# Optimization experiments

Measured on AMD Instinct MI355X. Metric: run time of the kernel, lower is better.

Reference implementation:

```python
import jax, jax.numpy as jnp
import numpy as np

BS, SEQ = 32, 48
VOCAB, H, IMG_F = 32529, 512, 4096
EPS = 1e-5


def setup_inputs() -> dict:
    key = jax.random.key(0)
    ks = jax.random.split(key, 24)
    stdv = 1.0 / np.sqrt(H)
    u = lambda k, shp, s=stdv: jax.random.uniform(k, shp, jnp.float32, -s, s)
    inp = {
        'img': jax.random.normal(ks[0], (BS, IMG_F), jnp.float32),
        'x': jax.random.randint(ks[1], (BS, SEQ), 0, VOCAB),
        # CNN (all convs are kernel-size-1 -> plain linears)
        'w1': u(ks[2], (2048, IMG_F)), 'b1': u(ks[3], (2048,)),
        'g1': jnp.ones((2048,)), 'be1': jnp.zeros((2048,)),
        'w2': u(ks[4], (1024, 2048)), 'b2': u(ks[5], (1024,)),
        'g2': jnp.ones((1024,)), 'be2': jnp.zeros((1024,)),
        'w3': u(ks[6], (H, 1024)), 'b3': u(ks[7], (H,)),
        'g3': jnp.ones((H,)), 'be3': jnp.zeros((H,)),
        # LSTM gates stacked in order i, f, g(c), o
        'U': u(ks[8], (H, 4 * H)),
        'V': u(ks[9], (H, 4 * H)),
        'bg': u(ks[10], (4 * H,)),
        'emb': u(ks[11], (VOCAB, H)),
        'Wout': u(ks[12], (H, VOCAB)),
        'bout': u(ks[13], (VOCAB,)),
    }
    return inp


def _bn(h, g, b):
    # BatchNorm1d in training mode over batch dim (spatial length is 1)
    mu = h.mean(0)
    v = jnp.var(h, 0)
    return g * (h - mu) * jax.lax.rsqrt(v + EPS) + b


def _cnn(img, w1, b1, g1, be1, w2, b2, g2, be2, w3, b3, g3, be3):
    h = jax.nn.relu(_bn(img @ w1.T + b1, g1, be1))
    h = jax.nn.relu(_bn(h @ w2.T + b2, g2, be2))
    h = jax.nn.relu(_bn(h @ w3.T + b3, g3, be3))
    return h  # [bs, 512]


def _lstm(feat, xe, U, V, bg):
    bs = feat.shape[0]
    h = jnp.zeros((bs, H), feat.dtype)
    c = jnp.zeros((bs, H), feat.dtype)

    def gates(z, c):
        z = z.reshape(bs, 4, H)
        i = jax.nn.sigmoid(z[:, 0])
        f = jax.nn.sigmoid(z[:, 1])
        g = jnp.tanh(z[:, 2])
        o = jax.nn.sigmoid(z[:, 3])
        c = f * c + i * g
        return o * jnp.tanh(c), c

    # image step: feat is added identically to every gate pre-activation
    z0 = feat[:, None, :].repeat(4, 1).reshape(bs, 4 * H) + h @ V + bg
    h, c = gates(z0, c)

    # precompute all input projections in one GEMM: [seq, bs, 4H]
    xU = jnp.einsum('bsh,hk->sbk', xe, U)

    def step(carry, xu):
        h, c = carry
        h, c = gates(xu + h @ V + bg, c)
        return (h, c), h

    (h, c), hs = jax.lax.scan(step, (h, c), xU)
    return hs.transpose(1, 0, 2), h, c  # [bs, seq, H]


def reference(img, x, w1, b1, g1, be1, w2, b2, g2, be2, w3, b3, g3, be3,
              U, V, bg, emb, Wout, bout):
    feat = _cnn(img, w1, b1, g1, be1, w2, b2, g2, be2, w3, b3, g3, be3)
    xe = emb[x]  # [bs, seq, H]
    hs, h, c = _lstm(feat, xe, U, V, bg)
    logits = hs @ Wout + bout  # [bs, seq, vocab]
    seq_pred = jax.nn.softmax(logits, axis=2)
    return seq_pred, (h, c)
```

## Files before the change

kernel.cpp:

```cpp
#include <hip/hip_runtime.h>
#include <stdint.h>

#define BS 32
#define SEQ 48
#define VOCAB 32529
#define HD 512
#define IMG_F 4096
#define EPS 1e-5f
#define NPAD16 2040

typedef __attribute__((ext_vector_type(8))) short short8;
typedef __attribute__((ext_vector_type(4))) float f32x4;

#define MFMA(a, b, c) __builtin_amdgcn_mfma_f32_16x16x32_bf16(a, b, c, 0, 0, 0)

static __device__ __forceinline__ unsigned short f2bf(float v) {
  union { float f; unsigned u; } c; c.f = v;
  unsigned r = (c.u + 0x7FFFu + ((c.u >> 16) & 1u)) >> 16;
  return (unsigned short)r;
}
static __device__ __forceinline__ float bf2f(unsigned short h) {
  union { unsigned u; float f; } c; c.u = ((unsigned)h) << 16; return c.f;
}
static __device__ __forceinline__ float sigf(float x) {
  x = fminf(fmaxf(x, -30.f), 30.f);
  return 1.f / (1.f + __expf(-x));
}
static __device__ __forceinline__ float tanh_(float x) {
  float t = __expf(fminf(fmaxf(2.f * x, -30.f), 30.f));
  return (t - 1.f) / (t + 1.f);
}

static __device__ __forceinline__ void gbar(unsigned* ctr, unsigned target) {
  __syncthreads();
  if (threadIdx.x == 0) {
    __threadfence();
    atomicAdd(ctr, 1u);
    while (atomicAdd(ctr, 0u) < target) __builtin_amdgcn_s_sleep(2);
  }
  __syncthreads();
  __threadfence();
}

__global__ __launch_bounds__(256) void k_gather(const float* __restrict__ emb,
                                                const int* __restrict__ x,
                                                unsigned short* __restrict__ xh,
                                                unsigned short* __restrict__ xl) {
  int idx = blockIdx.x * 256 + threadIdx.x;
  int m = idx >> 7;
  int k4 = (idx & 127) << 2;
  int t = m >> 5, b = m & 31;
  int row = x[b * SEQ + t];
  float4 v = *(const float4*)(emb + (size_t)row * HD + k4);
  float vv[4] = {v.x, v.y, v.z, v.w};
  unsigned short h_[4], l_[4];
#pragma unroll
  for (int i = 0; i < 4; ++i) {
    h_[i] = f2bf(vv[i]);
    l_[i] = f2bf(vv[i] - bf2f(h_[i]));
  }
  ushort4 hq = {h_[0], h_[1], h_[2], h_[3]};
  ushort4 lq = {l_[0], l_[1], l_[2], l_[3]};
  *(ushort4*)(xh + (size_t)m * HD + k4) = hq;
  *(ushort4*)(xl + (size_t)m * HD + k4) = lq;
}

__global__ __launch_bounds__(256) void k_pack(const float* __restrict__ W,
                                              unsigned short* __restrict__ Ph,
                                              unsigned short* __restrict__ Pl) {
  int f = blockIdx.x * 256 + threadIdx.x;
  int lane = f & 63;
  int kk = (f >> 6) & 15;
  int n16 = f >> 10;
  int c = n16 * 16 + (lane & 15);
  int k0 = kk * 32 + (lane >> 4) * 8;
  short8 oh, ol;
#pragma unroll
  for (int i = 0; i < 8; ++i) {
    float v = W[(size_t)(k0 + i) * 2048 + c];
    unsigned short hb = f2bf(v);
    oh[i] = (short)hb;
    ol[i] = (short)f2bf(v - bf2f(hb));
  }
  *(short8*)(Ph + (size_t)f * 8) = oh;
  *(short8*)(Pl + (size_t)f * 8) = ol;
}

__global__ __launch_bounds__(256) void k_packw(const float* __restrict__ W,
                                               unsigned short* __restrict__ P) {
  int f = blockIdx.x * 256 + threadIdx.x;
  int lane = f & 63;
  int kk = (f >> 6) & 15;
  int n16 = f >> 10;
  int c = n16 * 16 + (lane & 15);
  int k0 = kk * 32 + (lane >> 4) * 8;
  short8 o;
#pragma unroll
  for (int i = 0; i < 8; ++i) {
    float v = (c < VOCAB) ? W[(size_t)(k0 + i) * VOCAB + c] : 0.f;
    o[i] = (short)f2bf(v);
  }
  *(short8*)(P + (size_t)f * 8) = o;
}

template <int INF, int OUTF>
__global__ __launch_bounds__(256) void k_cnn(const float* __restrict__ in,
                                             const float* __restrict__ W,
                                             const float* __restrict__ gamma,
                                             const float* __restrict__ beta,
                                             float* __restrict__ out) {
  int tid = threadIdx.x;
  int b = tid & 31;
  int o = blockIdx.x * 8 + (tid >> 5);
  const float4* ip = (const float4*)(in + (size_t)b * INF);
  const float4* wp = (const float4*)(W + (size_t)o * INF);
  float a0 = 0, a1 = 0, a2 = 0, a3 = 0;
#pragma unroll 8
  for (int k = 0; k < INF / 4; ++k) {
    float4 a = ip[k], w = wp[k];
    a0 = fmaf(a.x, w.x, a0);
    a1 = fmaf(a.y, w.y, a1);
    a2 = fmaf(a.z, w.z, a2);
    a3 = fmaf(a.w, w.w, a3);
  }
  float pre = (a0 + a1) + (a2 + a3);
  float s = pre, q = pre * pre;
#pragma unroll
  for (int mk = 16; mk >= 1; mk >>= 1) {
    s += __shfl_xor(s, mk);
    q += __shfl_xor(q, mk);
  }
  float mu = s * (1.f / 32.f);
  float var = q * (1.f / 32.f) - mu * mu;
  float y = gamma[o] * (pre - mu) * rsqrtf(var + EPS) + beta[o];
  out[(size_t)b * OUTF + o] = fmaxf(y, 0.f);
}

__global__ __launch_bounds__(256) void k_xu(const unsigned short* __restrict__ xh,
                                            const unsigned short* __restrict__ xl,
                                            const unsigned short* __restrict__ Uh,
                                            const unsigned short* __restrict__ Ul,
                                            const float* __restrict__ bg,
                                            float* __restrict__ zx) {
  int mb = blockIdx.x;
  int nb = blockIdx.y;
  int w = threadIdx.x >> 6, l = threadIdx.x & 63;
  int lr = l & 15, lg = l >> 4;
  f32x4 acc[2][2] = {};
#pragma unroll 2
  for (int kk = 0; kk < 16; ++kk) {
    short8 ah[2], al[2];
#pragma unroll
    for (int m = 0; m < 2; ++m) {
      size_t ao = (size_t)(mb * 32 + m * 16 + lr) * HD + kk * 32 + lg * 8;
      ah[m] = *(const short8*)(xh + ao);
      al[m] = *(const short8*)(xl + ao);
    }
#pragma unroll
    for (int n = 0; n < 2; ++n) {
      int n16 = nb * 8 + w * 2 + n;
      size_t bo = ((size_t)(n16 * 16 + kk) * 64 + l) * 8;
      short8 bh = *(const short8*)(Uh + bo);
      short8 bl = *(const short8*)(Ul + bo);
#pragma unroll
      for (int m = 0; m < 2; ++m) {
        acc[m][n] = MFMA(ah[m], bh, acc[m][n]);
        acc[m][n] = MFMA(al[m], bh, acc[m][n]);
        acc[m][n] = MFMA(ah[m], bl, acc[m][n]);
      }
    }
  }
#pragma unroll
  for (int m = 0; m < 2; ++m)
#pragma unroll
    for (int n = 0; n < 2; ++n) {
      int col = (nb * 8 + w * 2 + n) * 16 + lr;
#pragma unroll
      for (int r = 0; r < 4; ++r) {
        int row = mb * 32 + m * 16 + lg * 4 + r;
        zx[(size_t)row * 2048 + col] = acc[m][n][r] + bg[col];
      }
    }
}

__global__ __launch_bounds__(256, 1) void k_lstm(
    const float* __restrict__ feat, const float* __restrict__ bg,
    const float* __restrict__ zx,
    const unsigned short* __restrict__ Vh, const unsigned short* __restrict__ Vl,
    unsigned short* __restrict__ hAh, unsigned short* __restrict__ hAl,
    unsigned short* __restrict__ hBh, unsigned short* __restrict__ hBl,
    unsigned short* __restrict__ hsb, float* __restrict__ hout,
    float* __restrict__ cout_, unsigned* __restrict__ barctr) {
  __shared__ float zsh[4][16][17];
  int blk = blockIdx.x;
  int mh = blk >> 5, nb = blk & 31;
  int tid = threadIdx.x;
  int w = tid >> 6, l = tid & 63, lr = l & 15, lg = l >> 4;
  int n16 = w * 32 + nb;
  short8 vh[16], vl[16];
#pragma unroll
  for (int kk = 0; kk < 16; ++kk) {
    size_t bo = ((size_t)(n16 * 16 + kk) * 64 + l) * 8;
    vh[kk] = *(const short8*)(Vh + bo);
    vl[kk] = *(const short8*)(Vl + bo);
  }
  int bl_ = tid >> 4, j = tid & 15;
  int b = mh * 16 + bl_, col = nb * 16 + j;
  int ci = b * HD + col;
  float fv = feat[ci];
  float c = sigf(fv + bg[col]) * tanh_(fv + bg[1024 + col]);
  float h = sigf(fv + bg[1536 + col]) * tanh_(c);
  {
    unsigned short hb_ = f2bf(h);
    hAh[ci] = hb_;
    hAl[ci] = f2bf(h - bf2f(hb_));
  }
  gbar(barctr, 64u);
  for (int t = 0; t < 48; ++t) {
    const unsigned short* ih = (t & 1) ? hBh : hAh;
    const unsigned short* il = (t & 1) ? hBl : hAl;
    unsigned short* oh = (t & 1) ? hAh : hBh;
    unsigned short* ol = (t & 1) ? hAl : hBl;
    const float* zr = zx + ((size_t)t * 32 + b) * 2048 + col;
    float z0p = zr[0], z1p = zr[512], z2p = zr[1024], z3p = zr[1536];
    f32x4 acc0 = {}, acc1 = {};
#pragma unroll
    for (int kk = 0; kk < 16; ++kk) {
      size_t ao = (size_t)(mh * 16 + lr) * HD + kk * 32 + lg * 8;
      short8 ah = *(const short8*)(ih + ao);
      short8 al = *(const short8*)(il + ao);
      if (kk & 1) {
        acc1 = MFMA(ah, vh[kk], acc1);
        acc1 = MFMA(al, vh[kk], acc1);
        acc1 = MFMA(ah, vl[kk], acc1);
      } else {
        acc0 = MFMA(ah, vh[kk], acc0);
        acc0 = MFMA(al, vh[kk], acc0);
        acc0 = MFMA(ah, vl[kk], acc0);
      }
    }
    f32x4 acc;
#pragma unroll
    for (int r = 0; r < 4; ++r) acc[r] = acc0[r] + acc1[r];
#pragma unroll
    for (int r = 0; r < 4; ++r) zsh[w][lg * 4 + r][lr] = acc[r];
    __syncthreads();
    float zi = zsh[0][bl_][j] + z0p;
    float zf = zsh[1][bl_][j] + z1p;
    float zg = zsh[2][bl_][j] + z2p;
    float zo = zsh[3][bl_][j] + z3p;
    c = sigf(zf) * c + sigf(zi) * tanh_(zg);
    h = sigf(zo) * tanh_(c);
    unsigned short hb2 = f2bf(h);
    oh[ci] = hb2;
    ol[ci] = f2bf(h - bf2f(hb2));
    hsb[((size_t)b * SEQ + t) * HD + col] = hb2;
    if (t < 47) gbar(barctr, 64u * (t + 2));
  }
  hout[ci] = h;
  cout_[ci] = c;
}

template <int MODE>
__global__ __launch_bounds__(256) void k_out(const unsigned short* __restrict__ A,
                                             const unsigned short* __restrict__ B,
                                             const float* __restrict__ bout,
                                             float* __restrict__ rowsum,
                                             float* __restrict__ dst) {
  int nb = blockIdx.x;
  int mb = blockIdx.y;
  int tid = threadIdx.x;
  int w = tid >> 6, l = tid & 63, lr = l & 15, lg = l >> 4;
  int wr = w >> 1, wc = w & 1;
  int mrow0 = mb * 128 + wr * 64;
  int n16_0 = nb * 8 + wc * 4;
  f32x4 acc[4][4] = {};
#pragma unroll 2
  for (int kk = 0; kk < 16; ++kk) {
    short8 a[4], bf[4];
#pragma unroll
    for (int mt = 0; mt < 4; ++mt)
      a[mt] = *(const short8*)(A + (size_t)(mrow0 + mt * 16 + lr) * HD + kk * 32 + lg * 8);
#pragma unroll
    for (int nt = 0; nt < 4; ++nt)
      bf[nt] = *(const short8*)(B + ((size_t)((n16_0 + nt) * 16 + kk) * 64 + l) * 8);
#pragma unroll
    for (int nt = 0; nt < 4; ++nt)
#pragma unroll
      for (int mt = 0; mt < 4; ++mt) acc[mt][nt] = MFMA(a[mt], bf[nt], acc[mt][nt]);
  }
#pragma unroll
  for (int mt = 0; mt < 4; ++mt) {
#pragma unroll
    for (int r = 0; r < 4; ++r) {
      int row = mrow0 + mt * 16 + lg * 4 + r;
      float inv = 1.f;
      if (MODE == 1) inv = 1.f / rowsum[row];
      float s = 0.f;
#pragma unroll
      for (int nt = 0; nt < 4; ++nt) {
        int col = (n16_0 + nt) * 16 + lr;
        bool valid = col < VOCAB;
        float e = __expf(acc[mt][nt][r] + (valid ? bout[col] : 0.f));
        if (MODE == 0) {
          s += valid ? e : 0.f;
        } else {
          if (valid) dst[(size_t)row * VOCAB + col] = e * inv;
        }
      }
      if (MODE == 0) {
        s += __shfl_xor(s, 1);
        s += __shfl_xor(s, 2);
        s += __shfl_xor(s, 4);
        s += __shfl_xor(s, 8);
        if (lr == 0) atomicAdd(&rowsum[row], s);
      }
    }
  }
}

extern "C" void kernel_launch(void* const* d_in, const int* in_sizes, int n_in,
                              void* d_out, int out_size, void* d_ws, size_t ws_size,
                              hipStream_t stream) {
  const float* img  = (const float*)d_in[0];
  const int*   x    = (const int*)d_in[1];
  const float* w1   = (const float*)d_in[2];
  const float* g1   = (const float*)d_in[4];
  const float* be1  = (const float*)d_in[5];
  const float* w2   = (const float*)d_in[6];
  const float* g2   = (const float*)d_in[8];
  const float* be2  = (const float*)d_in[9];
  const float* w3   = (const float*)d_in[10];
  const float* g3   = (const float*)d_in[12];
  const float* be3  = (const float*)d_in[13];
  const float* U    = (const float*)d_in[14];
  const float* V    = (const float*)d_in[15];
  const float* bg   = (const float*)d_in[16];
  const float* emb  = (const float*)d_in[17];
  const float* Wout = (const float*)d_in[18];
  const float* bout = (const float*)d_in[19];

  char* ws = (char*)d_ws;
  size_t off = 0;
  auto alloc = [&](size_t bytes) -> void* {
    void* p = ws + off;
    off = (off + bytes + 255) & ~(size_t)255;
    return p;
  };
  float* zx = (float*)alloc((size_t)48 * 32 * 2048 * 4);
  unsigned short* xh = (unsigned short*)alloc((size_t)1536 * 512 * 2);
  unsigned short* xl = (unsigned short*)alloc((size_t)1536 * 512 * 2);
  unsigned short* Uh = (unsigned short*)alloc((size_t)512 * 2048 * 2);
  unsigned short* Ul = (unsigned short*)alloc((size_t)512 * 2048 * 2);
  unsigned short* Vh = (unsigned short*)alloc((size_t)512 * 2048 * 2);
  unsigned short* Vl = (unsigned short*)alloc((size_t)512 * 2048 * 2);
  unsigned short* Wp = (unsigned short*)alloc((size_t)NPAD16 * 16 * 64 * 8 * 2);
  unsigned short* hAh = (unsigned short*)alloc(32 * 512 * 2);
  unsigned short* hAl = (unsigned short*)alloc(32 * 512 * 2);
  unsigned short* hBh = (unsigned short*)alloc(32 * 512 * 2);
  unsigned short* hBl = (unsigned short*)alloc(32 * 512 * 2);
  unsigned short* hsb = (unsigned short*)alloc((size_t)1536 * 512 * 2);
  float* feat = (float*)alloc(32 * 512 * 4);
  float* h1 = (float*)alloc(32 * 2048 * 4);
  float* h2 = (float*)alloc(32 * 1024 * 4);
  float* rowsum = (float*)alloc(1536 * 4);
  unsigned* barctr = (unsigned*)alloc(256);

  float* out = (float*)d_out;
  float* hout = out + 49964544;
  float* cout_ = out + 49964544 + 16384;

  k_gather<<<dim3(768), dim3(256), 0, stream>>>(emb, x, xh, xl);
  k_pack<<<dim3(512), dim3(256), 0, stream>>>(U, Uh, Ul);
  k_pack<<<dim3(512), dim3(256), 0, stream>>>(V, Vh, Vl);
  k_packw<<<dim3(8160), dim3(256), 0, stream>>>(Wout, Wp);
  k_cnn<4096, 2048><<<dim3(256), dim3(256), 0, stream>>>(img, w1, g1, be1, h1);
  k_cnn<2048, 1024><<<dim3(128), dim3(256), 0, stream>>>(h1, w2, g2, be2, h2);
  k_cnn<1024, 512><<<dim3(64), dim3(256), 0, stream>>>(h2, w3, g3, be3, feat);
  k_xu<<<dim3(48, 16), dim3(256), 0, stream>>>(xh, xl, Uh, Ul, bg, zx);
  hipMemsetAsync(barctr, 0, 256, stream);
  hipMemsetAsync(rowsum, 0, 1536 * 4, stream);
  k_lstm<<<dim3(64), dim3(256), 0, stream>>>(feat, bg, zx, Vh, Vl, hAh, hAl, hBh, hBl,
                                             hsb, hout, cout_, barctr);
  k_out<0><<<dim3(255, 12), dim3(256), 0, stream>>>(hsb, Wp, bout, rowsum, out);
  k_out<1><<<dim3(255, 12), dim3(256), 0, stream>>>(hsb, Wp, bout, rowsum, out);
}
```

Baseline: 1.662 ms.

## Restructure LSTM barrier, output GEMM tiling, and softmax into exp-store plus divide pass

The LSTM now runs 32 blocks of 512 threads, each covering all 32 batch rows, and uses a go-flag barrier instead of every block polling the shared counter. The output projection now reads a prepacked A fragment layout and uses larger tiles with B prefetch. It computes the GEMM once, storing bf16 exponentials and row sums, and a separate elementwise pass divides by the sums. This removes the second full GEMM pass. The cost is an extra ~100MB bf16 intermediate and some precision loss in the probabilities from rounding the exponentials to bf16.

```diff
diff --git a/kernel.cpp b/kernel.cpp
--- a/kernel.cpp
+++ b/kernel.cpp
@@ -7,7 +7,7 @@
 #define HD 512
 #define IMG_F 4096
 #define EPS 1e-5f
-#define NPAD16 2040
+#define NPAD16 2048
 
 typedef __attribute__((ext_vector_type(8))) short short8;
 typedef __attribute__((ext_vector_type(4))) float f32x4;
@@ -29,17 +29,6 @@
 static __device__ __forceinline__ float tanh_(float x) {
   float t = __expf(fminf(fmaxf(2.f * x, -30.f), 30.f));
   return (t - 1.f) / (t + 1.f);
-}
-
-static __device__ __forceinline__ void gbar(unsigned* ctr, unsigned target) {
-  __syncthreads();
-  if (threadIdx.x == 0) {
-    __threadfence();
-    atomicAdd(ctr, 1u);
-    while (atomicAdd(ctr, 0u) < target) __builtin_amdgcn_s_sleep(2);
-  }
-  __syncthreads();
-  __threadfence();
 }
 
 __global__ __launch_bounds__(256) void k_gather(const float* __restrict__ emb,
@@ -101,6 +90,18 @@
     o[i] = (short)f2bf(v);
   }
   *(short8*)(P + (size_t)f * 8) = o;
+}
+
+__global__ __launch_bounds__(256) void k_packa(const unsigned short* __restrict__ hsb,
+                                               unsigned short* __restrict__ Af) {
+  int f = blockIdx.x * 256 + threadIdx.x;
+  int lane = f & 63;
+  int kk = (f >> 6) & 15;
+  int m16 = f >> 10;
+  int row = m16 * 16 + (lane & 15);
+  int k0 = kk * 32 + (lane >> 4) * 8;
+  short8 v = *(const short8*)(hsb + (size_t)row * HD + k0);
+  *(short8*)(Af + (size_t)f * 8) = v;
 }
 
 template <int INF, int OUTF>
@@ -183,7 +184,23 @@
     }
 }
 
-__global__ __launch_bounds__(256, 1) void k_lstm(
+static __device__ __forceinline__ void gbar32(unsigned* ctr, unsigned* go, unsigned ep) {
+  __syncthreads();
+  if (threadIdx.x == 0) {
+    __threadfence();
+    unsigned prev = __hip_atomic_fetch_add(ctr, 1u, __ATOMIC_ACQ_REL, __HIP_MEMORY_SCOPE_AGENT);
+    if (prev == ep * 32u + 31u) {
+      __hip_atomic_store(go, ep + 1u, __ATOMIC_RELEASE, __HIP_MEMORY_SCOPE_AGENT);
+    } else {
+      while (__hip_atomic_load(go, __ATOMIC_ACQUIRE, __HIP_MEMORY_SCOPE_AGENT) < ep + 1u)
+        __builtin_amdgcn_s_sleep(1);
+    }
+  }
+  __syncthreads();
+  __threadfence();
+}
+
+__global__ __launch_bounds__(512, 1) void k_lstm(
     const float* __restrict__ feat, const float* __restrict__ bg,
     const float* __restrict__ zx,
     const unsigned short* __restrict__ Vh, const unsigned short* __restrict__ Vl,
@@ -191,21 +208,23 @@
     unsigned short* __restrict__ hBh, unsigned short* __restrict__ hBl,
     unsigned short* __restrict__ hsb, float* __restrict__ hout,
     float* __restrict__ cout_, unsigned* __restrict__ barctr) {
-  __shared__ float zsh[4][16][17];
-  int blk = blockIdx.x;
-  int mh = blk >> 5, nb = blk & 31;
+  __shared__ float zsh[4][32][17];
+  int nb = blockIdx.x;
   int tid = threadIdx.x;
   int w = tid >> 6, l = tid & 63, lr = l & 15, lg = l >> 4;
-  int n16 = w * 32 + nb;
+  int rt = w >> 2, g = w & 3;
+  int n16v = g * 32 + nb;
+  unsigned* ctr = barctr;
+  unsigned* go = barctr + 32;
   short8 vh[16], vl[16];
 #pragma unroll
   for (int kk = 0; kk < 16; ++kk) {
-    size_t bo = ((size_t)(n16 * 16 + kk) * 64 + l) * 8;
+    size_t bo = ((size_t)(n16v * 16 + kk) * 64 + l) * 8;
     vh[kk] = *(const short8*)(Vh + bo);
     vl[kk] = *(const short8*)(Vl + bo);
   }
-  int bl_ = tid >> 4, j = tid & 15;
-  int b = mh * 16 + bl_, col = nb * 16 + j;
+  int b = tid >> 4, j = tid & 15;
+  int col = nb * 16 + j;
   int ci = b * HD + col;
   float fv = feat[ci];
   float c = sigf(fv + bg[col]) * tanh_(fv + bg[1024 + col]);
@@ -215,7 +234,7 @@
     hAh[ci] = hb_;
     hAl[ci] = f2bf(h - bf2f(hb_));
   }
-  gbar(barctr, 64u);
+  gbar32(ctr, go, 0u);
   for (int t = 0; t < 48; ++t) {
     const unsigned short* ih = (t & 1) ? hBh : hAh;
     const unsigned short* il = (t & 1) ? hBl : hAl;
@@ -226,7 +245,7 @@
     f32x4 acc0 = {}, acc1 = {};
 #pragma unroll
     for (int kk = 0; kk < 16; ++kk) {
-      size_t ao = (size_t)(mh * 16 + lr) * HD + kk * 32 + lg * 8;
+      size_t ao = (size_t)(rt * 16 + lr) * HD + kk * 32 + lg * 8;
       short8 ah = *(const short8*)(ih + ao);
       short8 al = *(const short8*)(il + ao);
       if (kk & 1) {
@@ -239,84 +258,109 @@
         acc0 = MFMA(ah, vl[kk], acc0);
       }
     }
-    f32x4 acc;
-#pragma unroll
-    for (int r = 0; r < 4; ++r) acc[r] = acc0[r] + acc1[r];
-#pragma unroll
-    for (int r = 0; r < 4; ++r) zsh[w][lg * 4 + r][lr] = acc[r];
+#pragma unroll
+    for (int r = 0; r < 4; ++r) zsh[g][rt * 16 + lg * 4 + r][lr] = acc0[r] + acc1[r];
     __syncthreads();
-    float zi = zsh[0][bl_][j] + z0p;
-    float zf = zsh[1][bl_][j] + z1p;
-    float zg = zsh[2][bl_][j] + z2p;
-    float zo = zsh[3][bl_][j] + z3p;
+    float zi = zsh[0][b][j] + z0p;
+    float zf = zsh[1][b][j] + z1p;
+    float zg = zsh[2][b][j] + z2p;
+    float zo = zsh[3][b][j] + z3p;
     c = sigf(zf) * c + sigf(zi) * tanh_(zg);
     h = sigf(zo) * tanh_(c);
     unsigned short hb2 = f2bf(h);
     oh[ci] = hb2;
     ol[ci] = f2bf(h - bf2f(hb2));
     hsb[((size_t)b * SEQ + t) * HD + col] = hb2;
-    if (t < 47) gbar(barctr, 64u * (t + 2));
+    if (t < 47) gbar32(ctr, go, (unsigned)(t + 1));
   }
   hout[ci] = h;
   cout_[ci] = c;
 }
 
-template <int MODE>
-__global__ __launch_bounds__(256) void k_out(const unsigned short* __restrict__ A,
-                                             const unsigned short* __restrict__ B,
-                                             const float* __restrict__ bout,
-                                             float* __restrict__ rowsum,
-                                             float* __restrict__ dst) {
-  int nb = blockIdx.x;
-  int mb = blockIdx.y;
+__global__ __launch_bounds__(256, 2) void k_oute(const unsigned short* __restrict__ Af,
+                                                 const unsigned short* __restrict__ Wp,
+                                                 const float* __restrict__ bout,
+                                                 float* __restrict__ rowsum,
+                                                 unsigned short* __restrict__ expb) {
+  int mb = blockIdx.x;
+  int nb = blockIdx.y;
   int tid = threadIdx.x;
   int w = tid >> 6, l = tid & 63, lr = l & 15, lg = l >> 4;
   int wr = w >> 1, wc = w & 1;
   int mrow0 = mb * 128 + wr * 64;
-  int n16_0 = nb * 8 + wc * 4;
-  f32x4 acc[4][4] = {};
-#pragma unroll 2
+  int m16_0 = mrow0 >> 4;
+  int n16_0 = nb * 16 + wc * 8;
+  const short8* As = (const short8*)Af;
+  const short8* Bs = (const short8*)Wp;
+  f32x4 acc[4][8] = {};
+  short8 bcur[8], bnxt[8];
+#pragma unroll
+  for (int nt = 0; nt < 8; ++nt) bcur[nt] = Bs[((n16_0 + nt) * 16 + 0) * 64 + l];
+#pragma unroll
   for (int kk = 0; kk < 16; ++kk) {
-    short8 a[4], bf[4];
-#pragma unroll
-    for (int mt = 0; mt < 4; ++mt)
-      a[mt] = *(const short8*)(A + (size_t)(mrow0 + mt * 16 + lr) * HD + kk * 32 + lg * 8);
-#pragma unroll
-    for (int nt = 0; nt < 4; ++nt)
-      bf[nt] = *(const short8*)(B + ((size_t)((n16_0 + nt) * 16 + kk) * 64 + l) * 8);
-#pragma unroll
-    for (int nt = 0; nt < 4; ++nt)
-#pragma unroll
-      for (int mt = 0; mt < 4; ++mt) acc[mt][nt] = MFMA(a[mt], bf[nt], acc[mt][nt]);
+    short8 a[4];
+#pragma unroll
+    for (int mt = 0; mt < 4; ++mt) a[mt] = As[((m16_0 + mt) * 16 + kk) * 64 + l];
+    if (kk < 15) {
+#pragma unroll
+      for (int nt = 0; nt < 8; ++nt) bnxt[nt] = Bs[((n16_0 + nt) * 16 + kk + 1) * 64 + l];
+    }
+#pragma unroll
+    for (int nt = 0; nt < 8; ++nt)
+#pragma unroll
+      for (int mt = 0; mt < 4; ++mt) acc[mt][nt] = MFMA(a[mt], bcur[nt], acc[mt][nt]);
+#pragma unroll
+    for (int nt = 0; nt < 8; ++nt) bcur[nt] = bnxt[nt];
   }
 #pragma unroll
   for (int mt = 0; mt < 4; ++mt) {
 #pragma unroll
     for (int r = 0; r < 4; ++r) {
       int row = mrow0 + mt * 16 + lg * 4 + r;
-      float inv = 1.f;
-      if (MODE == 1) inv = 1.f / rowsum[row];
       float s = 0.f;
 #pragma unroll
-      for (int nt = 0; nt < 4; ++nt) {
+      for (int nt = 0; nt < 8; ++nt) {
         int col = (n16_0 + nt) * 16 + lr;
         bool valid = col < VOCAB;
         float e = __expf(acc[mt][nt][r] + (valid ? bout[col] : 0.f));
-        if (MODE == 0) {
-          s += valid ? e : 0.f;
-        } else {
-          if (valid) dst[(size_t)row * VOCAB + col] = e * inv;
+        if (valid) {
+          s += e;
+          expb[(size_t)row * VOCAB + col] = f2bf(e);
         }
       }
-      if (MODE == 0) {
-        s += __shfl_xor(s, 1);
-        s += __shfl_xor(s, 2);
-        s += __shfl_xor(s, 4);
-        s += __shfl_xor(s, 8);
-        if (lr == 0) atomicAdd(&rowsum[row], s);
-      }
-    }
-  }
+      s += __shfl_xor(s, 1);
+      s += __shfl_xor(s, 2);
+      s += __shfl_xor(s, 4);
+      s += __shfl_xor(s, 8);
+      if (lr == 0) atomicAdd(&rowsum[row], s);
+    }
+  }
+}
+
+__global__ __launch_bounds__(256) void k_div(const unsigned short* __restrict__ expb,
+                                             const float* __restrict__ rowsum,
+                                             float* __restrict__ out) {
+  unsigned i8 = (blockIdx.x * 256u + threadIdx.x) * 8u;
+  if (i8 >= 49964544u) return;
+  short8 e = *(const short8*)(expb + i8);
+  unsigned r0 = i8 / (unsigned)VOCAB;
+  unsigned r7 = (i8 + 7u) / (unsigned)VOCAB;
+  float o[8];
+  if (r0 == r7) {
+    float inv = 1.f / rowsum[r0];
+#pragma unroll
+    for (int i = 0; i < 8; ++i) o[i] = bf2f((unsigned short)e[i]) * inv;
+  } else {
+#pragma unroll
+    for (int i = 0; i < 8; ++i) {
+      unsigned rr = (i8 + i) / (unsigned)VOCAB;
+      o[i] = bf2f((unsigned short)e[i]) / rowsum[rr];
+    }
+  }
+  float4 o0 = {o[0], o[1], o[2], o[3]};
+  float4 o1 = {o[4], o[5], o[6], o[7]};
+  *(float4*)(out + i8) = o0;
+  *(float4*)(out + i8 + 4) = o1;
 }
 
 extern "C" void kernel_launch(void* const* d_in, const int* in_sizes, int n_in,
@@ -355,6 +399,7 @@
   unsigned short* Vh = (unsigned short*)alloc((size_t)512 * 2048 * 2);
   unsigned short* Vl = (unsigned short*)alloc((size_t)512 * 2048 * 2);
   unsigned short* Wp = (unsigned short*)alloc((size_t)NPAD16 * 16 * 64 * 8 * 2);
+  unsigned short* Af = (unsigned short*)alloc((size_t)96 * 16 * 64 * 8 * 2);
   unsigned short* hAh = (unsigned short*)alloc(32 * 512 * 2);
   unsigned short* hAl = (unsigned short*)alloc(32 * 512 * 2);
   unsigned short* hBh = (unsigned short*)alloc(32 * 512 * 2);
@@ -364,7 +409,8 @@
   float* h1 = (float*)alloc(32 * 2048 * 4);
   float* h2 = (float*)alloc(32 * 1024 * 4);
   float* rowsum = (float*)alloc(1536 * 4);
-  unsigned* barctr = (unsigned*)alloc(256);
+  unsigned* barctr = (unsigned*)alloc(512);
+  unsigned short* expb = (unsigned short*)alloc((size_t)49964544 * 2);
 
   float* out = (float*)d_out;
   float* hout = out + 49964544;
@@ -373,15 +419,16 @@
   k_gather<<<dim3(768), dim3(256), 0, stream>>>(emb, x, xh, xl);
   k_pack<<<dim3(512), dim3(256), 0, stream>>>(U, Uh, Ul);
   k_pack<<<dim3(512), dim3(256), 0, stream>>>(V, Vh, Vl);
-  k_packw<<<dim3(8160), dim3(256), 0, stream>>>(Wout, Wp);
+  k_packw<<<dim3(8192), dim3(256), 0, stream>>>(Wout, Wp);
   k_cnn<4096, 2048><<<dim3(256), dim3(256), 0, stream>>>(img, w1, g1, be1, h1);
   k_cnn<2048, 1024><<<dim3(128), dim3(256), 0, stream>>>(h1, w2, g2, be2, h2);
   k_cnn<1024, 512><<<dim3(64), dim3(256), 0, stream>>>(h2, w3, g3, be3, feat);
   k_xu<<<dim3(48, 16), dim3(256), 0, stream>>>(xh, xl, Uh, Ul, bg, zx);
-  hipMemsetAsync(barctr, 0, 256, stream);
+  hipMemsetAsync(barctr, 0, 512, stream);
   hipMemsetAsync(rowsum, 0, 1536 * 4, stream);
-  k_lstm<<<dim3(64), dim3(256), 0, stream>>>(feat, bg, zx, Vh, Vl, hAh, hAl, hBh, hBl,
+  k_lstm<<<dim3(32), dim3(512), 0, stream>>>(feat, bg, zx, Vh, Vl, hAh, hAl, hBh, hBl,
                                              hsb, hout, cout_, barctr);
-  k_out<0><<<dim3(255, 12), dim3(256), 0, stream>>>(hsb, Wp, bout, rowsum, out);
-  k_out<1><<<dim3(255, 12), dim3(256), 0, stream>>>(hsb, Wp, bout, rowsum, out);
-}
+  k_packa<<<dim3(384), dim3(256), 0, stream>>>(hsb, Af);
+  k_oute<<<dim3(12, 128), dim3(256), 0, stream>>>(Af, Wp, bout, rowsum, expb);
+  k_div<<<dim3(24397), dim3(256), 0, stream>>>(expb, rowsum, out);
+}
```

Measured after the change: 1.561 ms. 1.06x faster.
